# Performance work log

Measured on AMD Instinct MI355X. Metric: run time of the kernel, lower is better.

The kernel has to match this reference:

```python
import jax, jax.numpy as jnp
import numpy as np

HIDDEN = 1024
NUM_HEADS = 16
HEAD_DIM = HIDDEN // NUM_HEADS
BATCH = 2
SEQ = 2048


def setup_inputs() -> dict:
    key = jax.random.key(0)
    k1, k2, k3 = jax.random.split(key, 3)
    hidden_states = jax.random.normal(k1, (BATCH, SEQ, HIDDEN), dtype=jnp.float32)
    attention_mask = jnp.zeros((BATCH, 1, SEQ, SEQ), dtype=jnp.float32)
    # nn.Linear weights: stored as [out_features, in_features]
    w_qkv = jax.random.normal(k2, (3 * HIDDEN, HIDDEN), dtype=jnp.float32) * (HIDDEN ** -0.5)
    w_o = jax.random.normal(k3, (HIDDEN, HIDDEN), dtype=jnp.float32) * (HIDDEN ** -0.5)
    return {"hidden_states": hidden_states, "attention_mask": attention_mask,
            "w_qkv": w_qkv, "w_o": w_o}


def reference(hidden_states, attention_mask, w_qkv, w_o):
    B, S, H = hidden_states.shape
    scale = HEAD_DIM ** -0.5
    qkv = jnp.einsum('bsh,oh->bso', hidden_states, w_qkv)  # [B,S,3H]
    qkv = qkv.reshape(B, S, 3, NUM_HEADS, HEAD_DIM)
    q = qkv[:, :, 0].transpose(0, 2, 1, 3)  # [B,nH,S,hd]
    k = qkv[:, :, 1].transpose(0, 2, 1, 3)
    v = qkv[:, :, 2].transpose(0, 2, 1, 3)
    attn = jnp.einsum('bhqd,bhkd->bhqk', q, k) * scale
    attn = attn + attention_mask
    attn = jax.nn.softmax(attn, axis=-1)
    out = jnp.einsum('bhqk,bhkd->bhqd', attn, v)
    out = out.transpose(0, 2, 1, 3).reshape(B, S, H)
    return jnp.einsum('bsh,oh->bso', out, w_o)
```

## Files before the change

### kernel.cpp

```cpp
#include <hip/hip_runtime.h>

typedef unsigned short u16;
using bf16x8 = __attribute__((ext_vector_type(8))) __bf16;
using f32x4  = __attribute__((ext_vector_type(4))) float;
using u16x8  = __attribute__((ext_vector_type(8))) unsigned short;
using u16x4  = __attribute__((ext_vector_type(4))) unsigned short;

#define SEQ   2048
#define HID   1024
#define NHEAD 16
#define HD    64
#define BATCH 2
#define NTOK  4096

__device__ __forceinline__ u16 f2bf(float f) {
  unsigned u = __builtin_bit_cast(unsigned, f);
  u += 0x7fffu + ((u >> 16) & 1u);
  return (u16)(u >> 16);
}

__device__ __forceinline__ void gld_lds16(const void* g, void* l) {
  __builtin_amdgcn_global_load_lds(
      (__attribute__((address_space(1))) void*)(__UINTPTR_TYPE__)g,
      (__attribute__((address_space(3))) void*)l, 16, 0, 0);
}

__device__ __forceinline__ unsigned cvtpk(float lo, float hi) {
  unsigned r;
  asm("v_cvt_pk_bf16_f32 %0, %1, %2" : "=v"(r) : "v"(lo), "v"(hi));
  return r;
}

template<int CTRL>
__device__ __forceinline__ float row_ror(float x) {
  int xi = __builtin_bit_cast(int, x);
  int r  = __builtin_amdgcn_update_dpp(xi, xi, CTRL, 0xf, 0xf, false);
  return __builtin_bit_cast(float, r);
}
__device__ __forceinline__ float rowmax16(float x) {
  x = fmaxf(x, row_ror<0x121>(x));
  x = fmaxf(x, row_ror<0x122>(x));
  x = fmaxf(x, row_ror<0x124>(x));
  x = fmaxf(x, row_ror<0x128>(x));
  return x;
}
__device__ __forceinline__ float rowsum16(float x) {
  x += row_ror<0x121>(x);
  x += row_ror<0x122>(x);
  x += row_ror<0x124>(x);
  x += row_ror<0x128>(x);
  return x;
}

__global__ __launch_bounds__(256) void cvt3_kernel(const float* __restrict__ a, u16* __restrict__ oa,
                                                   const float* __restrict__ b, u16* __restrict__ ob,
                                                   const float* __restrict__ c, u16* __restrict__ oc) {
  const float* in; u16* out; int off;
  int bid = blockIdx.x;
  if (bid < 4096)      { in = a; out = oa; off = bid; }
  else if (bid < 7168) { in = b; out = ob; off = bid - 4096; }
  else                 { in = c; out = oc; off = bid - 7168; }
  int i = (off * 256 + threadIdx.x) * 4;
  float4 v = *reinterpret_cast<const float4*>(in + i);
  u16x4 o = { f2bf(v.x), f2bf(v.y), f2bf(v.z), f2bf(v.w) };
  *reinterpret_cast<u16x4*>(out + i) = o;
}

template<bool BF16OUT>
__global__ __launch_bounds__(256) void gemm_bt(const u16* __restrict__ A,
                                               const u16* __restrict__ B,
                                               void* __restrict__ Cv,
                                               u16* __restrict__ VT,
                                               int M, int N, int K) {
  __shared__ u16 At[128 * 64];
  __shared__ u16 Bt[128 * 64];
  const int tid  = threadIdx.x;
  const int wave = tid >> 6;
  const int lane = tid & 63;
  const int g    = lane >> 4;
  const int r16  = lane & 15;
  const int wr   = wave >> 1;
  const int wc   = wave & 1;
  const int bm   = blockIdx.y;
  const int bn   = blockIdx.x;
  const bool isV = (VT != nullptr) && (bn >= 16);

  const u16* Ab = A + (size_t)bm * 128 * K;
  const u16* Bb = B + (size_t)bn * 128 * K;
  const int srow = lane >> 3;
  const int scol = (lane & 7) * 8;

  f32x4 acc[4][4] = {};

  for (int kt = 0; kt < K; kt += 64) {
#pragma unroll
    for (int c = 0; c < 4; ++c) {
      int seg = wave * 4 + c;
      gld_lds16(Ab + (size_t)(seg * 8 + srow) * K + kt + scol, &At[seg * 512]);
      gld_lds16(Bb + (size_t)(seg * 8 + srow) * K + kt + scol, &Bt[seg * 512]);
    }
    __syncthreads();
#pragma unroll
    for (int ko = 0; ko < 64; ko += 32) {
      bf16x8 af[4], bfr[4];
#pragma unroll
      for (int mi = 0; mi < 4; ++mi)
        af[mi] = *reinterpret_cast<const bf16x8*>(&At[(wr * 64 + mi * 16 + r16) * 64 + ko + g * 8]);
#pragma unroll
      for (int ni = 0; ni < 4; ++ni)
        bfr[ni] = *reinterpret_cast<const bf16x8*>(&Bt[(wc * 64 + ni * 16 + r16) * 64 + ko + g * 8]);
      if (isV) {
#pragma unroll
        for (int mi = 0; mi < 4; ++mi)
#pragma unroll
          for (int ni = 0; ni < 4; ++ni)
            acc[ni][mi] = __builtin_amdgcn_mfma_f32_16x16x32_bf16(bfr[ni], af[mi], acc[ni][mi], 0, 0, 0);
      } else {
#pragma unroll
        for (int mi = 0; mi < 4; ++mi)
#pragma unroll
          for (int ni = 0; ni < 4; ++ni)
            acc[mi][ni] = __builtin_amdgcn_mfma_f32_16x16x32_bf16(af[mi], bfr[ni], acc[mi][ni], 0, 0, 0);
      }
    }
    __syncthreads();
  }

  if (isV) {
#pragma unroll
    for (int a = 0; a < 4; ++a)
#pragma unroll
      for (int c = 0; c < 4; ++c) {
#pragma unroll
        for (int r = 0; r < 4; ++r) {
          int hh   = (bn - 16) * 128 + wc * 64 + a * 16 + g * 4 + r;
          int tokg = bm * 128 + wr * 64 + c * 16 + r16;
          int b_   = tokg >> 11;
          int tok  = tokg & (SEQ - 1);
          int h_   = hh >> 6;
          int d_   = hh & 63;
          VT[((size_t)(b_ * NHEAD + h_) * HD + d_) * SEQ + tok] = f2bf(acc[a][c][r]);
        }
      }
  } else {
#pragma unroll
    for (int mi = 0; mi < 4; ++mi)
#pragma unroll
      for (int ni = 0; ni < 4; ++ni) {
        int row0 = bm * 128 + wr * 64 + mi * 16 + g * 4;
        int col  = bn * 128 + wc * 64 + ni * 16 + r16;
#pragma unroll
        for (int r = 0; r < 4; ++r) {
          float v = acc[mi][ni][r];
          if (BF16OUT) ((u16*)Cv)[(size_t)(row0 + r) * N + col] = f2bf(v);
          else         ((float*)Cv)[(size_t)(row0 + r) * N + col] = v;
        }
      }
  }
}

__global__ __launch_bounds__(256) void gemm_bt64(const u16* __restrict__ A,
                                                 const u16* __restrict__ B,
                                                 float* __restrict__ C,
                                                 int M, int N, int K) {
  __shared__ u16 At[128 * 64];
  __shared__ u16 Bt[64 * 64];
  const int tid  = threadIdx.x;
  const int wave = tid >> 6;
  const int lane = tid & 63;
  const int g    = lane >> 4;
  const int r16  = lane & 15;
  const int bm   = blockIdx.y;
  const int bn   = blockIdx.x;

  const u16* Ab = A + (size_t)bm * 128 * K;
  const u16* Bb = B + (size_t)bn * 64 * K;
  const int srow = lane >> 3;
  const int scol = (lane & 7) * 8;

  f32x4 acc[2][4] = {};

  for (int kt = 0; kt < K; kt += 64) {
#pragma unroll
    for (int c = 0; c < 4; ++c) {
      int seg = wave * 4 + c;
      gld_lds16(Ab + (size_t)(seg * 8 + srow) * K + kt + scol, &At[seg * 512]);
    }
#pragma unroll
    for (int c = 0; c < 2; ++c) {
      int seg = wave * 2 + c;
      gld_lds16(Bb + (size_t)(seg * 8 + srow) * K + kt + scol, &Bt[seg * 512]);
    }
    __syncthreads();
#pragma unroll
    for (int ko = 0; ko < 64; ko += 32) {
      bf16x8 af[2], bfr[4];
#pragma unroll
      for (int mi = 0; mi < 2; ++mi)
        af[mi] = *reinterpret_cast<const bf16x8*>(&At[(wave * 32 + mi * 16 + r16) * 64 + ko + g * 8]);
#pragma unroll
      for (int ni = 0; ni < 4; ++ni)
        bfr[ni] = *reinterpret_cast<const bf16x8*>(&Bt[(ni * 16 + r16) * 64 + ko + g * 8]);
#pragma unroll
      for (int mi = 0; mi < 2; ++mi)
#pragma unroll
        for (int ni = 0; ni < 4; ++ni)
          acc[mi][ni] = __builtin_amdgcn_mfma_f32_16x16x32_bf16(af[mi], bfr[ni], acc[mi][ni], 0, 0, 0);
    }
    __syncthreads();
  }

#pragma unroll
  for (int mi = 0; mi < 2; ++mi)
#pragma unroll
    for (int ni = 0; ni < 4; ++ni) {
      int row0 = bm * 128 + wave * 32 + mi * 16 + g * 4;
      int col  = bn * 64 + ni * 16 + r16;
#pragma unroll
      for (int r = 0; r < 4; ++r)
        C[(size_t)(row0 + r) * N + col] = acc[mi][ni][r];
    }
}

__global__ __launch_bounds__(256, 4) void attn_kernel(const u16* __restrict__ qkv,
                                                      const u16* __restrict__ VT,
                                                      const float* __restrict__ mask,
                                                      u16* __restrict__ AO) {
  __shared__ u16 Kt[2][64 * 64];
  __shared__ u16 Vt[2][64 * 64];
  __shared__ u16 Pl[4][16 * 64];

  const int tid  = threadIdx.x;
  const int w    = tid >> 6;
  const int lane = tid & 63;
  const int g    = lane >> 4;
  const int r16  = lane & 15;

  const int n  = blockIdx.x;
  const int x  = n & 7;
  const int s_ = n >> 3;
  const int h  = s_ & 15;
  const int t_ = ((s_ >> 4) << 3) + x;
  const int b  = t_ >> 5;
  const int qt = t_ & 31;

  const size_t tokbase = (size_t)b * SEQ;
  const u16* VTbh = VT + (size_t)(b * NHEAD + h) * HD * SEQ;

  bf16x8 aq[2];
  {
    int qrow = qt * 64 + w * 16 + r16;
#pragma unroll
    for (int ko = 0; ko < 2; ++ko)
      aq[ko] = *reinterpret_cast<const bf16x8*>(
          qkv + ((tokbase + qrow) * 3 + 0) * HID + h * HD + ko * 32 + g * 8);
  }

  f32x4 o[4] = {};
  float mrow[4], lrow[4];
#pragma unroll
  for (int r = 0; r < 4; ++r) { mrow[r] = -3.0e38f; lrow[r] = 0.f; }

  const int srowK = lane >> 3;

#define STAGE_K(buf, kb)                                                        \
  {                                                                             \
    _Pragma("unroll")                                                           \
    for (int c = 0; c < 2; ++c) {                                               \
      int seg = w * 2 + c;                                                      \
      int sK  = ((seg >> 1) + srowK) & 7;                                       \
      int srcc = (lane & 7) ^ sK;                                               \
      gld_lds16(qkv + ((tokbase + (kb) + seg * 8 + srowK) * 3 + 1) * HID +      \
                    h * HD + srcc * 8,                                          \
                &Kt[buf][seg * 512]);                                           \
    }                                                                           \
  }
#define STAGE_V(buf, kb)                                                        \
  {                                                                             \
    _Pragma("unroll")                                                           \
    for (int c = 0; c < 2; ++c) {                                               \
      int seg = w * 2 + c;                                                      \
      int sV  = ((seg >> 1) + srowK) & 7;                                       \
      int srcc = (lane & 7) ^ sV;                                               \
      gld_lds16(VTbh + (size_t)(seg * 8 + srowK) * SEQ + (kb) + srcc * 8,       \
                &Vt[buf][seg * 512]);                                           \
    }                                                                           \
  }

  STAGE_K(0, 0);
  STAGE_V(0, 0);

#pragma unroll 1
  for (int kb = 0; kb < SEQ; kb += 64) {
    const int cur = (kb >> 6) & 1;
    const int nxt = cur ^ 1;
    const bool more = (kb + 64) < SEQ;

    float mpre[4][4];
#pragma unroll
    for (int r = 0; r < 4; ++r) {
      int q = qt * 64 + w * 16 + g * 4 + r;
      const float* mp = mask + ((size_t)b * SEQ + q) * SEQ + kb;
#pragma unroll
      for (int ni = 0; ni < 4; ++ni) mpre[r][ni] = mp[ni * 16 + r16];
    }

    __syncthreads();

    f32x4 sf[4] = {};
    __builtin_amdgcn_s_setprio(1);
#pragma unroll
    for (int ko = 0; ko < 2; ++ko) {
      bf16x8 bk[4];
#pragma unroll
      for (int ni = 0; ni < 4; ++ni) {
        int row = ni * 16 + r16;
        int sK  = (ni + (r16 & 7)) & 7;
        bk[ni] = *reinterpret_cast<const bf16x8*>(
            &Kt[cur][row * 64 + (((ko * 4 + g) ^ sK) << 3)]);
      }
#pragma unroll
      for (int ni = 0; ni < 4; ++ni)
        sf[ni] = __builtin_amdgcn_mfma_f32_16x16x32_bf16(aq[ko], bk[ni], sf[ni], 0, 0, 0);
    }
    __builtin_amdgcn_s_setprio(0);

    float mx[4];
#pragma unroll
    for (int r = 0; r < 4; ++r) {
      float m_ = -3.0e38f;
#pragma unroll
      for (int ni = 0; ni < 4; ++ni) {
        float sv = sf[ni][r] * 0.125f + mpre[r][ni];
        sf[ni][r] = sv;
        m_ = fmaxf(m_, sv);
      }
      mx[r] = rowmax16(m_);
    }
    float need = 0.f;
#pragma unroll
    for (int r = 0; r < 4; ++r) need = fmaxf(need, mx[r] - mrow[r]);
    if (__any(need > 8.0f)) {
#pragma unroll
      for (int r = 0; r < 4; ++r) {
        float mnew  = fmaxf(mrow[r], mx[r]);
        float alpha = __expf(mrow[r] - mnew);
        mrow[r] = mnew;
        lrow[r] *= alpha;
#pragma unroll
        for (int di = 0; di < 4; ++di) o[di][r] *= alpha;
      }
    }
#pragma unroll
    for (int r = 0; r < 4; ++r) {
      float p0 = __expf(sf[0][r] - mrow[r]);
      float p1 = __expf(sf[1][r] - mrow[r]);
      float p2 = __expf(sf[2][r] - mrow[r]);
      float p3 = __expf(sf[3][r] - mrow[r]);
      float s  = rowsum16(p0 + p1 + p2 + p3);
      lrow[r] += s;
      unsigned pk01 = cvtpk(p0, p1);
      unsigned pk23 = cvtpk(p2, p3);
      int prow = g * 4 + r;
      int sP   = prow & 7;
      u16 pv[4] = { (u16)pk01, (u16)(pk01 >> 16), (u16)pk23, (u16)(pk23 >> 16) };
#pragma unroll
      for (int ni = 0; ni < 4; ++ni) {
        int chunk = ni * 2 + (r16 >> 3);
        Pl[w][prow * 64 + ((chunk ^ sP) << 3) + (r16 & 7)] = pv[ni];
      }
    }

    if (more) { STAGE_K(nxt, kb + 64); STAGE_V(nxt, kb + 64); }

    __builtin_amdgcn_s_setprio(1);
#pragma unroll
    for (int kk = 0; kk < 2; ++kk) {
      bf16x8 pa, bv[4];
      pa = *reinterpret_cast<const bf16x8*>(
          &Pl[w][r16 * 64 + (((kk * 4 + g) ^ (r16 & 7)) << 3)]);
#pragma unroll
      for (int di = 0; di < 4; ++di) {
        int row = di * 16 + r16;
        int sV  = (di + (r16 & 7)) & 7;
        bv[di] = *reinterpret_cast<const bf16x8*>(
            &Vt[cur][row * 64 + (((kk * 4 + g) ^ sV) << 3)]);
      }
#pragma unroll
      for (int di = 0; di < 4; ++di)
        o[di] = __builtin_amdgcn_mfma_f32_16x16x32_bf16(pa, bv[di], o[di], 0, 0, 0);
    }
    __builtin_amdgcn_s_setprio(0);
  }

#pragma unroll
  for (int di = 0; di < 4; ++di)
#pragma unroll
    for (int r = 0; r < 4; ++r) {
      int srow = qt * 64 + w * 16 + g * 4 + r;
      float val = o[di][r] / lrow[r];
      AO[(tokbase + srow) * HID + h * HD + di * 16 + r16] = f2bf(val);
    }
#undef STAGE_K
#undef STAGE_V
}

extern "C" void kernel_launch(void* const* d_in, const int* in_sizes, int n_in,
                              void* d_out, int out_size, void* d_ws, size_t ws_size,
                              hipStream_t stream) {
  (void)in_sizes; (void)n_in; (void)out_size; (void)ws_size;
  const float* hs   = (const float*)d_in[0];
  const float* mask = (const float*)d_in[1];
  const float* wqkv = (const float*)d_in[2];
  const float* wo   = (const float*)d_in[3];
  float* out = (float*)d_out;

  char* ws   = (char*)d_ws;
  u16* Xb    = (u16*)(ws);
  u16* Wqkvb = (u16*)(ws + 8u  * 1024 * 1024);
  u16* Wob   = (u16*)(ws + 14u * 1024 * 1024);
  u16* QKVb  = (u16*)(ws + 16u * 1024 * 1024);
  u16* AOb   = (u16*)(ws + 40u * 1024 * 1024);
  u16* VT    = (u16*)(ws + 48u * 1024 * 1024);

  cvt3_kernel<<<8192, 256, 0, stream>>>(hs, Xb, wqkv, Wqkvb, wo, Wob);

  gemm_bt<true><<<dim3(3072 / 128, 4096 / 128), 256, 0, stream>>>(Xb, Wqkvb, QKVb, VT, NTOK, 3072, HID);
  attn_kernel  <<<1024, 256, 0, stream>>>(QKVb, VT, mask, AOb);
  gemm_bt64    <<<dim3(1024 / 64, 4096 / 128), 256, 0, stream>>>(AOb, Wob, out, NTOK, 1024, HID);
}
```

Before: 169.2 us.

## Split attention KV range in two halves with 512-thread blocks and merge kernel

The attention kernel now uses 8 waves per block covering 128 query rows, and splits the key/value sequence into two halves handled by separate blocks (split-KV). Partial outputs go to AO and into the unused V slot of the QKV buffer, with row max and sum stored to a scratch array. A new merge kernel then combines the two halves with log-sum-exp weights. The change trades extra global traffic, an added launch and bf16 rounding of the partial results for a different work split, and it relies on the V region being dead after VT has been written.

```diff
diff --git a/kernel.cpp b/kernel.cpp
--- a/kernel.cpp
+++ b/kernel.cpp
@@ -17,6 +17,10 @@
   unsigned u = __builtin_bit_cast(unsigned, f);
   u += 0x7fffu + ((u >> 16) & 1u);
   return (u16)(u >> 16);
+}
+__device__ __forceinline__ float bf2f(u16 v) {
+  unsigned u = ((unsigned)v) << 16;
+  return __builtin_bit_cast(float, u);
 }
 
 __device__ __forceinline__ void gld_lds16(const void* g, void* l) {
@@ -222,13 +226,15 @@
     }
 }
 
-__global__ __launch_bounds__(256, 4) void attn_kernel(const u16* __restrict__ qkv,
-                                                      const u16* __restrict__ VT,
-                                                      const float* __restrict__ mask,
-                                                      u16* __restrict__ AO) {
+__global__ __launch_bounds__(512) void attn_kernel(const u16* __restrict__ qkv,
+                                                   const u16* __restrict__ VT,
+                                                   const float* __restrict__ mask,
+                                                   u16* __restrict__ P0,
+                                                   u16* __restrict__ P1,
+                                                   float* __restrict__ ML) {
   __shared__ u16 Kt[2][64 * 64];
   __shared__ u16 Vt[2][64 * 64];
-  __shared__ u16 Pl[4][16 * 64];
+  __shared__ u16 Pl[8][16 * 64];
 
   const int tid  = threadIdx.x;
   const int w    = tid >> 6;
@@ -236,20 +242,25 @@
   const int g    = lane >> 4;
   const int r16  = lane & 15;
 
-  const int n  = blockIdx.x;
+  const int n0   = blockIdx.x;
+  const int half = n0 >> 9;
+  const int n    = n0 & 511;
+  const int kv0  = half << 10;
+  const int KVEND = kv0 + 1024;
+
   const int x  = n & 7;
   const int s_ = n >> 3;
   const int h  = s_ & 15;
   const int t_ = ((s_ >> 4) << 3) + x;
-  const int b  = t_ >> 5;
-  const int qt = t_ & 31;
+  const int b  = t_ >> 4;
+  const int qt = t_ & 15;
 
   const size_t tokbase = (size_t)b * SEQ;
   const u16* VTbh = VT + (size_t)(b * NHEAD + h) * HD * SEQ;
 
   bf16x8 aq[2];
   {
-    int qrow = qt * 64 + w * 16 + r16;
+    int qrow = qt * 128 + w * 16 + r16;
 #pragma unroll
     for (int ko = 0; ko < 2; ++ko)
       aq[ko] = *reinterpret_cast<const bf16x8*>(
@@ -265,41 +276,33 @@
 
 #define STAGE_K(buf, kb)                                                        \
   {                                                                             \
-    _Pragma("unroll")                                                           \
-    for (int c = 0; c < 2; ++c) {                                               \
-      int seg = w * 2 + c;                                                      \
-      int sK  = ((seg >> 1) + srowK) & 7;                                       \
-      int srcc = (lane & 7) ^ sK;                                               \
-      gld_lds16(qkv + ((tokbase + (kb) + seg * 8 + srowK) * 3 + 1) * HID +      \
-                    h * HD + srcc * 8,                                          \
-                &Kt[buf][seg * 512]);                                           \
-    }                                                                           \
+    int sK  = ((w >> 1) + srowK) & 7;                                           \
+    int srcc = (lane & 7) ^ sK;                                                 \
+    gld_lds16(qkv + ((tokbase + (kb) + w * 8 + srowK) * 3 + 1) * HID +          \
+                  h * HD + srcc * 8,                                            \
+              &Kt[buf][w * 512]);                                               \
   }
 #define STAGE_V(buf, kb)                                                        \
   {                                                                             \
-    _Pragma("unroll")                                                           \
-    for (int c = 0; c < 2; ++c) {                                               \
-      int seg = w * 2 + c;                                                      \
-      int sV  = ((seg >> 1) + srowK) & 7;                                       \
-      int srcc = (lane & 7) ^ sV;                                               \
-      gld_lds16(VTbh + (size_t)(seg * 8 + srowK) * SEQ + (kb) + srcc * 8,       \
-                &Vt[buf][seg * 512]);                                           \
-    }                                                                           \
-  }
-
-  STAGE_K(0, 0);
-  STAGE_V(0, 0);
+    int sV  = ((w >> 1) + srowK) & 7;                                           \
+    int srcc = (lane & 7) ^ sV;                                                 \
+    gld_lds16(VTbh + (size_t)(w * 8 + srowK) * SEQ + (kb) + srcc * 8,           \
+              &Vt[buf][w * 512]);                                               \
+  }
+
+  STAGE_K(0, kv0);
+  STAGE_V(0, kv0);
 
 #pragma unroll 1
-  for (int kb = 0; kb < SEQ; kb += 64) {
+  for (int kb = kv0; kb < KVEND; kb += 64) {
     const int cur = (kb >> 6) & 1;
     const int nxt = cur ^ 1;
-    const bool more = (kb + 64) < SEQ;
+    const bool more = (kb + 64) < KVEND;
 
     float mpre[4][4];
 #pragma unroll
     for (int r = 0; r < 4; ++r) {
-      int q = qt * 64 + w * 16 + g * 4 + r;
+      int q = qt * 128 + w * 16 + g * 4 + r;
       const float* mp = mask + ((size_t)b * SEQ + q) * SEQ + kb;
 #pragma unroll
       for (int ni = 0; ni < 4; ++ni) mpre[r][ni] = mp[ni * 16 + r16];
@@ -397,12 +400,49 @@
   for (int di = 0; di < 4; ++di)
 #pragma unroll
     for (int r = 0; r < 4; ++r) {
-      int srow = qt * 64 + w * 16 + g * 4 + r;
+      int srow = qt * 128 + w * 16 + g * 4 + r;
+      size_t idx = tokbase + srow;
       float val = o[di][r] / lrow[r];
-      AO[(tokbase + srow) * HID + h * HD + di * 16 + r16] = f2bf(val);
-    }
+      u16 bv = f2bf(val);
+      if (half == 0) P0[idx * HID + h * HD + di * 16 + r16] = bv;
+      else           P1[(idx * 3 + 2) * HID + h * HD + di * 16 + r16] = bv;
+    }
+  if (r16 == 0) {
+#pragma unroll
+    for (int r = 0; r < 4; ++r) {
+      int srow = qt * 128 + w * 16 + g * 4 + r;
+      size_t mi_ = ((tokbase + srow) * NHEAD + h) * 4 + half * 2;
+      ML[mi_ + 0] = mrow[r];
+      ML[mi_ + 1] = lrow[r];
+    }
+  }
 #undef STAGE_K
 #undef STAGE_V
+}
+
+__global__ __launch_bounds__(256) void merge_kernel(u16* __restrict__ P0,
+                                                    const u16* __restrict__ P1,
+                                                    const float* __restrict__ ML) {
+  int t  = blockIdx.x * 256 + threadIdx.x;
+  int i  = t >> 3;
+  int d0 = (t & 7) * 8;
+  int tok = i >> 4, h = i & 15;
+  size_t off0 = (size_t)tok * HID + h * 64 + d0;
+  size_t off1 = ((size_t)tok * 3 + 2) * HID + h * 64 + d0;
+  float m0 = ML[(size_t)i * 4 + 0], l0 = ML[(size_t)i * 4 + 1];
+  float m1 = ML[(size_t)i * 4 + 2], l1 = ML[(size_t)i * 4 + 3];
+  float ms = fmaxf(m0, m1);
+  float w0 = l0 * __expf(m0 - ms);
+  float w1 = l1 * __expf(m1 - ms);
+  float inv = 1.0f / (w0 + w1);
+  w0 *= inv; w1 *= inv;
+  u16x8 a = *reinterpret_cast<const u16x8*>(P0 + off0);
+  u16x8 c = *reinterpret_cast<const u16x8*>(P1 + off1);
+  u16x8 o;
+#pragma unroll
+  for (int j = 0; j < 8; ++j)
+    o[j] = f2bf(w0 * bf2f((u16)a[j]) + w1 * bf2f((u16)c[j]));
+  *reinterpret_cast<u16x8*>(P0 + off0) = o;
 }
 
 extern "C" void kernel_launch(void* const* d_in, const int* in_sizes, int n_in,
@@ -422,10 +462,12 @@
   u16* QKVb  = (u16*)(ws + 16u * 1024 * 1024);
   u16* AOb   = (u16*)(ws + 40u * 1024 * 1024);
   u16* VT    = (u16*)(ws + 48u * 1024 * 1024);
+  float* ML  = (float*)(ws + 56u * 1024 * 1024);
 
   cvt3_kernel<<<8192, 256, 0, stream>>>(hs, Xb, wqkv, Wqkvb, wo, Wob);
 
   gemm_bt<true><<<dim3(3072 / 128, 4096 / 128), 256, 0, stream>>>(Xb, Wqkvb, QKVb, VT, NTOK, 3072, HID);
-  attn_kernel  <<<1024, 256, 0, stream>>>(QKVb, VT, mask, AOb);
+  attn_kernel  <<<1024, 512, 0, stream>>>(QKVb, VT, mask, AOb, QKVb, ML);
+  merge_kernel <<<2048, 256, 0, stream>>>(AOb, QKVb, ML);
   gemm_bt64    <<<dim3(1024 / 64, 4096 / 128), 256, 0, stream>>>(AOb, Wob, out, NTOK, 1024, HID);
 }
```

New measurement: 172.3 us. No clear change (+1.8%).
